# Kernel tuning notes

Hardware: AMD Instinct MI355X
Metric: run time of the kernel (lower is better)

The kernel has to match this reference:

```python
import jax, jax.numpy as jnp
import numpy as np

NUM_HEADS = 16
HEAD_SIZE = 64
D_MODEL = NUM_HEADS * HEAD_SIZE  # 1024


def setup_inputs() -> dict:
    key = jax.random.key(0)
    ks = jax.random.split(key, 12)
    B, S = 4, 2048
    q = jax.random.normal(ks[0], (B, S, D_MODEL), dtype=jnp.float32)
    k = jax.random.normal(ks[1], (B, S, D_MODEL), dtype=jnp.float32)
    v = jax.random.normal(ks[2], (B, S, D_MODEL), dtype=jnp.float32)
    w = jax.random.uniform(ks[3], (B, S), dtype=jnp.float32)
    scale = 1.0 / np.sqrt(D_MODEL)
    Wq = jax.random.normal(ks[4], (D_MODEL, D_MODEL), dtype=jnp.float32) * scale
    Wk = jax.random.normal(ks[5], (D_MODEL, D_MODEL), dtype=jnp.float32) * scale
    Wv = jax.random.normal(ks[6], (D_MODEL, D_MODEL), dtype=jnp.float32) * scale
    Wo = jax.random.normal(ks[7], (D_MODEL, D_MODEL), dtype=jnp.float32) * scale
    bq = jnp.zeros((D_MODEL,), jnp.float32)
    bk = jnp.zeros((D_MODEL,), jnp.float32)
    bv = jnp.zeros((D_MODEL,), jnp.float32)
    bo = jnp.zeros((D_MODEL,), jnp.float32)
    return {"q": q, "k": k, "v": v, "w": w,
            "Wq": Wq, "bq": bq, "Wk": Wk, "bk": bk,
            "Wv": Wv, "bv": bv, "Wo": Wo, "bo": bo}


def reference(q, k, v, w, Wq, bq, Wk, bk, Wv, bv, Wo, bo):
    B, S, _ = q.shape
    H, Dh = NUM_HEADS, HEAD_SIZE

    def split_heads(x):  # [B,S,D] -> [B,H,S,Dh]
        return x.reshape(B, -1, H, Dh).transpose(0, 2, 1, 3)

    q_h = split_heads(q @ Wq + bq)
    k_h = split_heads(k @ Wk + bk)
    v_h = split_heads(v @ Wv + bv)

    # [B,H,Sq,Sk]
    score = jnp.einsum('bhqd,bhkd->bhqk', q_h, k_h) / jnp.sqrt(
        jnp.asarray(Dh, jnp.float32))
    # weighted unnormalized softmax: exp(score)*w / sum (no max subtraction,
    # faithful to original)
    exp_score = jnp.exp(score) * w[:, None, None, :]
    attn = exp_score / (jnp.sum(exp_score, axis=-1, keepdims=True) + 1e-12)

    context = jnp.einsum('bhqk,bhkd->bhqd', attn, v_h)  # [B,H,S,Dh]
    context = context.transpose(0, 2, 1, 3).reshape(B, -1, H * Dh)
    return context @ Wo + bo
```

## Files before the change

### kernel.cpp

```cpp
#include <hip/hip_runtime.h>
#include <hip/hip_bf16.h>

typedef __bf16 bf16x8 __attribute__((ext_vector_type(8)));
typedef float f32x4 __attribute__((ext_vector_type(4)));
typedef float f32x8 __attribute__((ext_vector_type(8)));
typedef float f32x16 __attribute__((ext_vector_type(16)));
typedef unsigned short u16;
typedef unsigned int u32;

#define SB 4
#define SS 2048
#define SD 1024
#define SH 16
#define SDH 64

__device__ __forceinline__ u16 f2bf(float f) {
  union { float f; u32 u; } x; x.f = f;
  u32 r = (x.u + 0x7FFFu + ((x.u >> 16) & 1u)) >> 16;
  return (u16)r;
}

__device__ __forceinline__ void gl_lds16(const void* g, void* l) {
  __builtin_amdgcn_global_load_lds(
      (__attribute__((address_space(1))) void*)g,
      (__attribute__((address_space(3))) void*)l, 16, 0, 0);
}

__global__ void cast3_kernel(const float* __restrict__ q,
                             const float* __restrict__ k,
                             const float* __restrict__ v,
                             u32* __restrict__ oq, u32* __restrict__ ok,
                             u32* __restrict__ ov) {
  int sel = blockIdx.y;
  const float* in = (sel == 0) ? q : (sel == 1) ? k : v;
  u32* out = (sel == 0) ? oq : (sel == 1) ? ok : ov;
  int i = blockIdx.x * 256 + threadIdx.x;
  const float4* inp = (const float4*)in;
  float4 a = inp[2 * i], b = inp[2 * i + 1];
  uint4 o;
  asm("v_cvt_pk_bf16_f32 %0, %1, %2" : "=v"(o.x) : "v"(a.x), "v"(a.y));
  asm("v_cvt_pk_bf16_f32 %0, %1, %2" : "=v"(o.y) : "v"(a.z), "v"(a.w));
  asm("v_cvt_pk_bf16_f32 %0, %1, %2" : "=v"(o.z) : "v"(b.x), "v"(b.y));
  asm("v_cvt_pk_bf16_f32 %0, %1, %2" : "=v"(o.w) : "v"(b.z), "v"(b.w));
  ((uint4*)out)[i] = o;
}

__global__ void log2w_kernel(const float* __restrict__ w,
                             float* __restrict__ lwg) {
  int i = blockIdx.x * 256 + threadIdx.x;
  lwg[i] = __builtin_amdgcn_logf(w[i]);
}

__global__ void transpose_cast_kernel(const float* __restrict__ W0,
                                      const float* __restrict__ W1,
                                      const float* __restrict__ W2,
                                      const float* __restrict__ W3,
                                      u16* __restrict__ T0,
                                      u16* __restrict__ T1,
                                      u16* __restrict__ T2,
                                      u16* __restrict__ T3) {
  __shared__ float t[32][33];
  int z = blockIdx.z;
  const float* W = (z == 0) ? W0 : (z == 1) ? W1 : (z == 2) ? W2 : W3;
  u16* Wt = (z == 0) ? T0 : (z == 1) ? T1 : (z == 2) ? T2 : T3;
  int bx = blockIdx.x, by = blockIdx.y;
  int tx = threadIdx.x, ty = threadIdx.y;
#pragma unroll
  for (int j = 0; j < 32; j += 8)
    t[ty + j][tx] = W[(size_t)(by * 32 + ty + j) * SD + bx * 32 + tx];
  __syncthreads();
#pragma unroll
  for (int j = 0; j < 32; j += 8)
    Wt[(size_t)(bx * 32 + ty + j) * SD + by * 32 + tx] = f2bf(t[tx][ty + j]);
}

template <int MODE>
__global__ __launch_bounds__(256, 2)
void gemm_bt(const u16* __restrict__ A, const u16* __restrict__ Bt,
             const float* __restrict__ bias, void* __restrict__ Out,
             int M, int N, int K) {
  __shared__ u16 Asl[2][128 * 64];
  __shared__ u16 Bsl[2][128 * 64];
  const int ntile = N >> 7;
  int bid = blockIdx.x;
  bid = (bid & 7) * ((int)gridDim.x >> 3) + (bid >> 3);
  int m0 = (bid / ntile) * 128, n0 = (bid % ntile) * 128;
  int tid = threadIdx.x;
  int lane = tid & 63, wv = tid >> 6;
  int wr = wv >> 1, wc = wv & 1;

  auto stage = [&](int buf, int k0) {
#pragma unroll
    for (int it = 0; it < 4; ++it) {
      int c = tid + it * 256;
      int row = c >> 3, sl = c & 7;
      int ssl = sl ^ (row & 7);
      gl_lds16(A + (size_t)(m0 + row) * K + k0 + ssl * 8,
               (char*)&Asl[buf][0] + c * 16);
      gl_lds16(Bt + (size_t)(n0 + row) * K + k0 + ssl * 8,
               (char*)&Bsl[buf][0] + c * 16);
    }
  };

  f32x4 acc[4][4] = {};
  stage(0, 0);

  int nk = K >> 6;
  for (int kt = 0; kt < nk; ++kt) {
    int buf = kt & 1;
    if (kt + 1 < nk) {
      stage(buf ^ 1, (kt + 1) << 6);
      asm volatile("s_waitcnt vmcnt(8) lgkmcnt(0)" ::: "memory");
    } else {
      asm volatile("s_waitcnt vmcnt(0) lgkmcnt(0)" ::: "memory");
    }
    __builtin_amdgcn_s_barrier();
#pragma unroll
    for (int kk = 0; kk < 2; ++kk) {
      bf16x8 af[4], bfr[4];
#pragma unroll
      for (int i = 0; i < 4; ++i) {
        int ar = wr * 64 + i * 16 + (lane & 15);
        int abyt = (ar * 128 + (kk * 32 + (lane >> 4) * 8) * 2) ^
                   ((ar & 7) << 4);
        af[i] = *(const bf16x8*)((const char*)&Asl[buf][0] + abyt);
        int br = wc * 64 + i * 16 + (lane & 15);
        int bbyt = (br * 128 + (kk * 32 + (lane >> 4) * 8) * 2) ^
                   ((br & 7) << 4);
        bfr[i] = *(const bf16x8*)((const char*)&Bsl[buf][0] + bbyt);
      }
#pragma unroll
      for (int i = 0; i < 4; ++i)
#pragma unroll
        for (int j = 0; j < 4; ++j)
          acc[i][j] = __builtin_amdgcn_mfma_f32_16x16x32_bf16(
              af[i], bfr[j], acc[i][j], 0, 0, 0);
    }
    __builtin_amdgcn_s_barrier();
  }

  int cg = lane >> 4, cc = lane & 15;
#pragma unroll
  for (int i = 0; i < 4; ++i) {
#pragma unroll
    for (int j = 0; j < 4; ++j) {
#pragma unroll
      for (int r = 0; r < 4; ++r) {
        int m = m0 + wr * 64 + i * 16 + cg * 4 + r;
        int n = n0 + wc * 64 + j * 16 + cc;
        float val = acc[i][j][r];
        if (MODE == 0) {
          val = (val + bias[n]) * 0.18033688011112042f;
          int b = m >> 11, s = m & 2047, h = n >> 6, dh = n & 63;
          ((u16*)Out)[((size_t)((b * SH + h) * SS + s) << 6) + dh] = f2bf(val);
        } else if (MODE == 1) {
          val += bias[n];
          int b = m >> 11, s = m & 2047, h = n >> 6, dh = n & 63;
          size_t off = ((size_t)(b * SH + h) << 17) + ((size_t)(s >> 5) << 11) +
                       ((size_t)(dh >> 4) << 9) +
                       ((size_t)((s & 31) | ((dh & 8) << 2)) << 3) + (dh & 7);
          ((u16*)Out)[off] = f2bf(val);
        } else if (MODE == 2) {
          val += bias[m];
          int h = m >> 6, dh = m & 63, b = n >> 11, s = n & 2047;
          size_t off = ((size_t)(b * SH + h) << 17) + ((size_t)(s >> 4) << 10) +
                       ((size_t)(dh >> 5) << 9) +
                       ((size_t)(((s >> 3) & 1) * 32 + (dh & 31)) << 3) +
                       (s & 7);
          ((u16*)Out)[off] = f2bf(val);
        } else {
          val += bias[n];
          ((float*)Out)[(size_t)m * N + n] = val;
        }
      }
    }
  }
}

__global__ __launch_bounds__(256, 4)
void attn_kernel(const u16* __restrict__ Qh, const u16* __restrict__ Kf,
                 const u16* __restrict__ Vf, const float* __restrict__ lwg,
                 u16* __restrict__ Ctx) {
  __shared__ u16 Kl[2][4096];
  __shared__ u16 Vl[2][4096];
  __shared__ float lwl[SS];

  int bid = blockIdx.x;
  int swz = (bid & 7) * 128 + (bid >> 3);
  int bh = swz >> 4;
  int qt = swz & 15;
  int b = bh >> 4, hh = bh & 15;
  int q0 = qt * 128;
  int tid = threadIdx.x, lane = tid & 63, qw = tid >> 6;
  int ql = lane & 31, h = lane >> 5;
  const size_t basebh = (size_t)bh * (SS * SDH);
  const char* Ksrc = (const char*)(Kf + basebh);
  const char* Vsrc = (const char*)(Vf + basebh);

  {
    const float4* src = (const float4*)(lwg + b * SS);
    float4 r0 = src[tid];
    float4 r1 = src[tid + 256];
    ((float4*)lwl)[tid] = r0;
    ((float4*)lwl)[tid + 256] = r1;
  }

  bf16x8 qf[4];
  {
    const u16* qp = Qh + basebh + (size_t)(q0 + qw * 32 + ql) * SDH + h * 8;
#pragma unroll
    for (int st = 0; st < 4; ++st) qf[st] = *(const bf16x8*)(qp + st * 16);
  }

  auto stageK = [&](int s, int t) {
    const char* p = Ksrc + (size_t)t * 8192;
    gl_lds16(p + tid * 16, (char*)&Kl[s][0] + tid * 16);
    gl_lds16(p + 4096 + tid * 16, (char*)&Kl[s][0] + 4096 + tid * 16);
  };
  auto stageV = [&](int s, int t) {
    const char* p = Vsrc + (size_t)t * 8192;
    gl_lds16(p + tid * 16, (char*)&Vl[s][0] + tid * 16);
    gl_lds16(p + 4096 + tid * 16, (char*)&Vl[s][0] + 4096 + tid * 16);
  };

  f32x16 ctx0 = {}, ctx1 = {};
  float rs = 0.f;
  u32 pk[8][2];

  auto qk = [&](int t) {
    const char* Ks = (const char*)&Kl[t & 1][0];
    int kvb = t * 64;
#pragma unroll
    for (int kt = 0; kt < 2; ++kt) {
      bf16x8 kf[4];
#pragma unroll
      for (int st = 0; st < 4; ++st)
        kf[st] = *(const bf16x8*)(Ks + (kt * 4 + st) * 1024 + lane * 16);
      const float* lb = lwl + kvb + kt * 32 + h * 4;
      f32x4 l0 = *(const f32x4*)(lb);
      f32x4 l1 = *(const f32x4*)(lb + 8);
      f32x4 l2 = *(const f32x4*)(lb + 16);
      f32x4 l3 = *(const f32x4*)(lb + 24);
      f32x8 lo = __builtin_shufflevector(l0, l1, 0, 1, 2, 3, 4, 5, 6, 7);
      f32x8 hi = __builtin_shufflevector(l2, l3, 0, 1, 2, 3, 4, 5, 6, 7);
      f32x16 sc = __builtin_shufflevector(lo, hi, 0, 1, 2, 3, 4, 5, 6, 7, 8,
                                          9, 10, 11, 12, 13, 14, 15);
      __builtin_amdgcn_s_setprio(1);
#pragma unroll
      for (int st = 0; st < 4; ++st)
        sc = __builtin_amdgcn_mfma_f32_32x32x16_bf16(kf[st], qf[st], sc,
                                                     0, 0, 0);
      __builtin_amdgcn_s_setprio(0);
#pragma unroll
      for (int e2 = 0; e2 < 4; ++e2) {
        float v0 = __builtin_amdgcn_exp2f(sc[e2 * 4 + 0]);
        float v1 = __builtin_amdgcn_exp2f(sc[e2 * 4 + 1]);
        float v2 = __builtin_amdgcn_exp2f(sc[e2 * 4 + 2]);
        float v3 = __builtin_amdgcn_exp2f(sc[e2 * 4 + 3]);
        rs += (v0 + v1) + (v2 + v3);
        u32 p0, p1;
        asm("v_cvt_pk_bf16_f32 %0, %1, %2" : "=v"(p0) : "v"(v0), "v"(v1));
        asm("v_cvt_pk_bf16_f32 %0, %1, %2" : "=v"(p1) : "v"(v2), "v"(v3));
        pk[kt * 4 + e2][0] = p0;
        pk[kt * 4 + e2][1] = p1;
      }
    }
  };

  auto pv = [&](int t) {
    const char* Vs = (const char*)&Vl[t & 1][0];
#pragma unroll
    for (int ksl = 0; ksl < 4; ++ksl) {
      bf16x8 vf0 = *(const bf16x8*)(Vs + (ksl * 2 + 0) * 1024 + lane * 16);
      bf16x8 vf1 = *(const bf16x8*)(Vs + (ksl * 2 + 1) * 1024 + lane * 16);
      u32 d0 = pk[2 * ksl][0], d1 = pk[2 * ksl][1];
      u32 s0 = pk[2 * ksl + 1][0], s1 = pk[2 * ksl + 1][1];
      asm("v_permlane32_swap_b32 %0, %1" : "+v"(d0), "+v"(s0));
      asm("v_permlane32_swap_b32 %0, %1" : "+v"(d1), "+v"(s1));
      union { u32 uu[4]; bf16x8 v; } pa;
      pa.uu[0] = d0; pa.uu[1] = d1; pa.uu[2] = s0; pa.uu[3] = s1;
      __builtin_amdgcn_s_setprio(1);
      ctx0 = __builtin_amdgcn_mfma_f32_32x32x16_bf16(pa.v, vf0, ctx0, 0, 0, 0);
      ctx1 = __builtin_amdgcn_mfma_f32_32x32x16_bf16(pa.v, vf1, ctx1, 0, 0, 0);
      __builtin_amdgcn_s_setprio(0);
    }
  };

  stageK(0, 0);
  stageV(0, 0);
  asm volatile("s_waitcnt lgkmcnt(0)" ::: "memory");
  __builtin_amdgcn_s_barrier();

  for (int t = 0; t < 31; ++t) {
    asm volatile("s_waitcnt vmcnt(2)" ::: "memory");
    __builtin_amdgcn_s_barrier();
    stageK((t + 1) & 1, t + 1);
    stageV((t + 1) & 1, t + 1);
    qk(t);
    asm volatile("s_waitcnt vmcnt(4)" ::: "memory");
    pv(t);
  }
  asm volatile("s_waitcnt vmcnt(2)" ::: "memory");
  __builtin_amdgcn_s_barrier();
  qk(31);
  asm volatile("s_waitcnt vmcnt(0)" ::: "memory");
  pv(31);

  rs += __shfl_xor(rs, 32, 64);
  float rinv = 1.0f / (rs + 1e-12f);
#pragma unroll
  for (int reg = 0; reg < 16; ++reg) {
    int qrow = (reg & 3) + 8 * (reg >> 2) + 4 * h;
    float ri = __shfl(rinv, qrow, 64);
    int srow = q0 + qw * 32 + qrow;
    size_t base = ((size_t)(b * SS + srow) << 10) + hh * SDH;
    Ctx[base + ql] = f2bf(ctx0[reg] * ri);
    Ctx[base + 32 + ql] = f2bf(ctx1[reg] * ri);
  }
}

extern "C" void kernel_launch(void* const* d_in, const int* in_sizes, int n_in,
                              void* d_out, int out_size, void* d_ws,
                              size_t ws_size, hipStream_t stream) {
  const float* q = (const float*)d_in[0];
  const float* k = (const float*)d_in[1];
  const float* v = (const float*)d_in[2];
  const float* w = (const float*)d_in[3];
  const float* Wq = (const float*)d_in[4];
  const float* bq = (const float*)d_in[5];
  const float* Wk = (const float*)d_in[6];
  const float* bk = (const float*)d_in[7];
  const float* Wv = (const float*)d_in[8];
  const float* bv = (const float*)d_in[9];
  const float* Wo = (const float*)d_in[10];
  const float* bo = (const float*)d_in[11];
  float* out = (float*)d_out;

  char* ws = (char*)d_ws;
  const size_t SZ = (size_t)8192 * 1024 * 2;
  u16* qb = (u16*)(ws);
  u16* kb = (u16*)(ws + SZ);
  u16* vb = (u16*)(ws + 2 * SZ);
  u16* WqT = (u16*)(ws + 3 * SZ);
  u16* WkT = WqT + 1024 * 1024;
  u16* WvT = WkT + 1024 * 1024;
  u16* WoT = WvT + 1024 * 1024;
  u16* Qh = (u16*)(ws + 3 * SZ + (size_t)4 * 1024 * 1024 * 2);
  u16* Kf = Qh + (size_t)8192 * 1024;
  u16* Vf = Kf + (size_t)8192 * 1024;
  float* lwg = (float*)(ws + 3 * SZ + (size_t)4 * 1024 * 1024 * 2 +
                        (size_t)3 * 8192 * 1024 * 2);
  u16* Ctx = qb;

  cast3_kernel<<<dim3(4096, 3), 256, 0, stream>>>(q, k, v, (u32*)qb,
                                                  (u32*)kb, (u32*)vb);
  log2w_kernel<<<32, 256, 0, stream>>>(w, lwg);
  dim3 tb(32, 8), tg(32, 32, 4);
  transpose_cast_kernel<<<tg, tb, 0, stream>>>(Wq, Wk, Wv, Wo,
                                               WqT, WkT, WvT, WoT);

  gemm_bt<0><<<512, 256, 0, stream>>>(qb, WqT, bq, Qh, 8192, 1024, 1024);
  gemm_bt<1><<<512, 256, 0, stream>>>(kb, WkT, bk, Kf, 8192, 1024, 1024);
  gemm_bt<2><<<512, 256, 0, stream>>>(WvT, vb, bv, Vf, 1024, 8192, 1024);

  attn_kernel<<<1024, 256, 0, stream>>>(Qh, Kf, Vf, lwg, Ctx);

  gemm_bt<3><<<512, 256, 0, stream>>>(Ctx, WoT, bo, out, 8192, 1024, 1024);
}
```

Measured before the change: 214.3 us.

## Software-pipeline attention: overlap softmax of tile t with PV of tile t-1

Restructures the attention loop so QK for tile t runs, then the exp/convert softmax for tile t is interleaved with the PV MFMAs of tile t-1, using double-buffered probability registers and a triple-buffered V LDS ring. The goal is to hide transcendental and VALU latency under matrix-core work. In exchange it uses more LDS (an extra V buffer) and more registers, and launch bounds drop to 3 blocks per CU, which lowers occupancy.

New measurement: 219.4 us. +2.4%, slower.

```diff
diff --git a/kernel.cpp b/kernel.cpp
--- a/kernel.cpp
+++ b/kernel.cpp
@@ -177,12 +177,12 @@
   }
 }
 
-__global__ __launch_bounds__(256, 4)
+__global__ __launch_bounds__(256, 3)
 void attn_kernel(const u16* __restrict__ Qh, const u16* __restrict__ Kf,
                  const u16* __restrict__ Vf, const float* __restrict__ lwg,
                  u16* __restrict__ Ctx) {
   __shared__ u16 Kl[2][4096];
-  __shared__ u16 Vl[2][4096];
+  __shared__ u16 Vl[3][4096];
   __shared__ float lwl[SS];
 
   int bid = blockIdx.x;
@@ -225,10 +225,9 @@
 
   f32x16 ctx0 = {}, ctx1 = {};
   float rs = 0.f;
-  u32 pk[8][2];
-
-  auto qk = [&](int t) {
-    const char* Ks = (const char*)&Kl[t & 1][0];
+  u32 pkA[8][2], pkB[8][2];
+
+  auto qk = [&](const char* Ks, int t, f32x16& s0v, f32x16& s1v) {
     int kvb = t * 64;
 #pragma unroll
     for (int kt = 0; kt < 2; ++kt) {
@@ -251,30 +250,38 @@
         sc = __builtin_amdgcn_mfma_f32_32x32x16_bf16(kf[st], qf[st], sc,
                                                      0, 0, 0);
       __builtin_amdgcn_s_setprio(0);
-#pragma unroll
-      for (int e2 = 0; e2 < 4; ++e2) {
-        float v0 = __builtin_amdgcn_exp2f(sc[e2 * 4 + 0]);
-        float v1 = __builtin_amdgcn_exp2f(sc[e2 * 4 + 1]);
-        float v2 = __builtin_amdgcn_exp2f(sc[e2 * 4 + 2]);
-        float v3 = __builtin_amdgcn_exp2f(sc[e2 * 4 + 3]);
-        rs += (v0 + v1) + (v2 + v3);
-        u32 p0, p1;
-        asm("v_cvt_pk_bf16_f32 %0, %1, %2" : "=v"(p0) : "v"(v0), "v"(v1));
-        asm("v_cvt_pk_bf16_f32 %0, %1, %2" : "=v"(p1) : "v"(v2), "v"(v3));
-        pk[kt * 4 + e2][0] = p0;
-        pk[kt * 4 + e2][1] = p1;
-      }
-    }
-  };
-
-  auto pv = [&](int t) {
-    const char* Vs = (const char*)&Vl[t & 1][0];
+      if (kt == 0) s0v = sc; else s1v = sc;
+    }
+  };
+
+#define SM_SLICE(sidx, scv)                                                 \
+  {                                                                         \
+    float v0 = __builtin_amdgcn_exp2f((scv)[((sidx) & 3) * 4 + 0]);         \
+    float v1 = __builtin_amdgcn_exp2f((scv)[((sidx) & 3) * 4 + 1]);         \
+    float v2 = __builtin_amdgcn_exp2f((scv)[((sidx) & 3) * 4 + 2]);         \
+    float v3 = __builtin_amdgcn_exp2f((scv)[((sidx) & 3) * 4 + 3]);         \
+    rs += (v0 + v1) + (v2 + v3);                                            \
+    asm("v_cvt_pk_bf16_f32 %0, %1, %2"                                      \
+        : "=v"(pkN[sidx][0]) : "v"(v0), "v"(v1));                           \
+    asm("v_cvt_pk_bf16_f32 %0, %1, %2"                                      \
+        : "=v"(pkN[sidx][1]) : "v"(v2), "v"(v3));                           \
+  }
+
+  auto region2 = [&](f32x16& s0v, f32x16& s1v, u32 (&pkN)[8][2],
+                     u32 (&pkO)[8][2], const char* Vs) {
 #pragma unroll
     for (int ksl = 0; ksl < 4; ++ksl) {
       bf16x8 vf0 = *(const bf16x8*)(Vs + (ksl * 2 + 0) * 1024 + lane * 16);
       bf16x8 vf1 = *(const bf16x8*)(Vs + (ksl * 2 + 1) * 1024 + lane * 16);
-      u32 d0 = pk[2 * ksl][0], d1 = pk[2 * ksl][1];
-      u32 s0 = pk[2 * ksl + 1][0], s1 = pk[2 * ksl + 1][1];
+      if (ksl < 2) {
+        SM_SLICE(2 * ksl + 0, s0v);
+        SM_SLICE(2 * ksl + 1, s0v);
+      } else {
+        SM_SLICE(2 * ksl + 0, s1v);
+        SM_SLICE(2 * ksl + 1, s1v);
+      }
+      u32 d0 = pkO[2 * ksl][0], d1 = pkO[2 * ksl][1];
+      u32 s0 = pkO[2 * ksl + 1][0], s1 = pkO[2 * ksl + 1][1];
       asm("v_permlane32_swap_b32 %0, %1" : "+v"(d0), "+v"(s0));
       asm("v_permlane32_swap_b32 %0, %1" : "+v"(d1), "+v"(s1));
       union { u32 uu[4]; bf16x8 v; } pa;
@@ -286,25 +293,60 @@
     }
   };
 
+  auto smx_only = [&](f32x16& s0v, f32x16& s1v, u32 (&pkN)[8][2]) {
+#pragma unroll
+    for (int sidx = 0; sidx < 8; ++sidx) {
+      if (sidx < 4) SM_SLICE(sidx, s0v) else SM_SLICE(sidx, s1v);
+    }
+  };
+  auto pv_only = [&](u32 (&pkO)[8][2], const char* Vs) {
+#pragma unroll
+    for (int ksl = 0; ksl < 4; ++ksl) {
+      bf16x8 vf0 = *(const bf16x8*)(Vs + (ksl * 2 + 0) * 1024 + lane * 16);
+      bf16x8 vf1 = *(const bf16x8*)(Vs + (ksl * 2 + 1) * 1024 + lane * 16);
+      u32 d0 = pkO[2 * ksl][0], d1 = pkO[2 * ksl][1];
+      u32 s0 = pkO[2 * ksl + 1][0], s1 = pkO[2 * ksl + 1][1];
+      asm("v_permlane32_swap_b32 %0, %1" : "+v"(d0), "+v"(s0));
+      asm("v_permlane32_swap_b32 %0, %1" : "+v"(d1), "+v"(s1));
+      union { u32 uu[4]; bf16x8 v; } pa;
+      pa.uu[0] = d0; pa.uu[1] = d1; pa.uu[2] = s0; pa.uu[3] = s1;
+      ctx0 = __builtin_amdgcn_mfma_f32_32x32x16_bf16(pa.v, vf0, ctx0, 0, 0, 0);
+      ctx1 = __builtin_amdgcn_mfma_f32_32x32x16_bf16(pa.v, vf1, ctx1, 0, 0, 0);
+    }
+  };
+
+  f32x16 sc0, sc1;
+
   stageK(0, 0);
   stageV(0, 0);
-  asm volatile("s_waitcnt lgkmcnt(0)" ::: "memory");
+  asm volatile("s_waitcnt vmcnt(2) lgkmcnt(0)" ::: "memory");
   __builtin_amdgcn_s_barrier();
-
-  for (int t = 0; t < 31; ++t) {
+  stageK(1, 1);
+  stageV(1, 1);
+  qk((const char*)&Kl[0][0], 0, sc0, sc1);
+  smx_only(sc0, sc1, pkA);
+
+  for (int t = 1; t <= 29; t += 2) {
     asm volatile("s_waitcnt vmcnt(2)" ::: "memory");
     __builtin_amdgcn_s_barrier();
     stageK((t + 1) & 1, t + 1);
-    stageV((t + 1) & 1, t + 1);
-    qk(t);
-    asm volatile("s_waitcnt vmcnt(4)" ::: "memory");
-    pv(t);
+    stageV((t + 1) % 3, t + 1);
+    qk((const char*)&Kl[t & 1][0], t, sc0, sc1);
+    region2(sc0, sc1, pkB, pkA, (const char*)&Vl[(t - 1) % 3][0]);
+    asm volatile("s_waitcnt vmcnt(2)" ::: "memory");
+    __builtin_amdgcn_s_barrier();
+    stageK((t + 2) & 1, t + 2);
+    stageV((t + 2) % 3, t + 2);
+    qk((const char*)&Kl[(t + 1) & 1][0], t + 1, sc0, sc1);
+    region2(sc0, sc1, pkA, pkB, (const char*)&Vl[t % 3][0]);
   }
   asm volatile("s_waitcnt vmcnt(2)" ::: "memory");
   __builtin_amdgcn_s_barrier();
-  qk(31);
+  qk((const char*)&Kl[1][0], 31, sc0, sc1);
+  region2(sc0, sc1, pkB, pkA, (const char*)&Vl[30 % 3][0]);
   asm volatile("s_waitcnt vmcnt(0)" ::: "memory");
-  pv(31);
+  pv_only(pkB, (const char*)&Vl[31 % 3][0]);
+#undef SM_SLICE
 
   rs += __shfl_xor(rs, 32, 64);
   float rinv = 1.0f / (rs + 1e-12f);
```

## Merge prep kernels into one launch and halve GEMM K-tile for occupancy

Applied to the files above, without the earlier changes.

Folds the cast, log-weight and weight transpose-cast kernels into a single prep kernel dispatched by block index, removing two launches. The GEMM K-tile shrinks from 64 to 32, halving LDS per block, and launch bounds are raised to allow three blocks per CU. A new swizzle packs two rows per 128-byte LDS line. The trade is more K iterations and barriers per tile in exchange for higher occupancy and fewer launches.

After: 222.6 us. +3.9%, slower.

```diff
diff --git a/kernel.cpp b/kernel.cpp
--- a/kernel.cpp
+++ b/kernel.cpp
@@ -26,61 +26,60 @@
       (__attribute__((address_space(3))) void*)l, 16, 0, 0);
 }
 
-__global__ void cast3_kernel(const float* __restrict__ q,
-                             const float* __restrict__ k,
-                             const float* __restrict__ v,
-                             u32* __restrict__ oq, u32* __restrict__ ok,
-                             u32* __restrict__ ov) {
-  int sel = blockIdx.y;
-  const float* in = (sel == 0) ? q : (sel == 1) ? k : v;
-  u32* out = (sel == 0) ? oq : (sel == 1) ? ok : ov;
-  int i = blockIdx.x * 256 + threadIdx.x;
-  const float4* inp = (const float4*)in;
-  float4 a = inp[2 * i], b = inp[2 * i + 1];
-  uint4 o;
-  asm("v_cvt_pk_bf16_f32 %0, %1, %2" : "=v"(o.x) : "v"(a.x), "v"(a.y));
-  asm("v_cvt_pk_bf16_f32 %0, %1, %2" : "=v"(o.y) : "v"(a.z), "v"(a.w));
-  asm("v_cvt_pk_bf16_f32 %0, %1, %2" : "=v"(o.z) : "v"(b.x), "v"(b.y));
-  asm("v_cvt_pk_bf16_f32 %0, %1, %2" : "=v"(o.w) : "v"(b.z), "v"(b.w));
-  ((uint4*)out)[i] = o;
-}
-
-__global__ void log2w_kernel(const float* __restrict__ w,
-                             float* __restrict__ lwg) {
-  int i = blockIdx.x * 256 + threadIdx.x;
-  lwg[i] = __builtin_amdgcn_logf(w[i]);
-}
-
-__global__ void transpose_cast_kernel(const float* __restrict__ W0,
-                                      const float* __restrict__ W1,
-                                      const float* __restrict__ W2,
-                                      const float* __restrict__ W3,
-                                      u16* __restrict__ T0,
-                                      u16* __restrict__ T1,
-                                      u16* __restrict__ T2,
-                                      u16* __restrict__ T3) {
+__global__ void prep_kernel(const float* __restrict__ q,
+                            const float* __restrict__ k,
+                            const float* __restrict__ v,
+                            u32* __restrict__ oq, u32* __restrict__ ok,
+                            u32* __restrict__ ov,
+                            const float* __restrict__ w,
+                            float* __restrict__ lwg,
+                            const float* __restrict__ W0,
+                            const float* __restrict__ W1,
+                            const float* __restrict__ W2,
+                            const float* __restrict__ W3,
+                            u16* __restrict__ T0, u16* __restrict__ T1,
+                            u16* __restrict__ T2, u16* __restrict__ T3) {
   __shared__ float t[32][33];
-  int z = blockIdx.z;
-  const float* W = (z == 0) ? W0 : (z == 1) ? W1 : (z == 2) ? W2 : W3;
-  u16* Wt = (z == 0) ? T0 : (z == 1) ? T1 : (z == 2) ? T2 : T3;
-  int bx = blockIdx.x, by = blockIdx.y;
-  int tx = threadIdx.x, ty = threadIdx.y;
-#pragma unroll
-  for (int j = 0; j < 32; j += 8)
-    t[ty + j][tx] = W[(size_t)(by * 32 + ty + j) * SD + bx * 32 + tx];
-  __syncthreads();
-#pragma unroll
-  for (int j = 0; j < 32; j += 8)
-    Wt[(size_t)(bx * 32 + ty + j) * SD + by * 32 + tx] = f2bf(t[tx][ty + j]);
+  int bid = blockIdx.x, tid = threadIdx.x;
+  if (bid < 12288) {
+    int sel = bid >> 12;
+    int i = (bid & 4095) * 256 + tid;
+    const float* in = (sel == 0) ? q : (sel == 1) ? k : v;
+    u32* out = (sel == 0) ? oq : (sel == 1) ? ok : ov;
+    const float4* inp = (const float4*)in;
+    float4 a = inp[2 * i], b = inp[2 * i + 1];
+    uint4 o;
+    asm("v_cvt_pk_bf16_f32 %0, %1, %2" : "=v"(o.x) : "v"(a.x), "v"(a.y));
+    asm("v_cvt_pk_bf16_f32 %0, %1, %2" : "=v"(o.y) : "v"(a.z), "v"(a.w));
+    asm("v_cvt_pk_bf16_f32 %0, %1, %2" : "=v"(o.z) : "v"(b.x), "v"(b.y));
+    asm("v_cvt_pk_bf16_f32 %0, %1, %2" : "=v"(o.w) : "v"(b.z), "v"(b.w));
+    ((uint4*)out)[i] = o;
+  } else if (bid < 16384) {
+    int local = bid - 12288;
+    int z = local >> 10, by = (local >> 5) & 31, bx = local & 31;
+    const float* W = (z == 0) ? W0 : (z == 1) ? W1 : (z == 2) ? W2 : W3;
+    u16* Wt = (z == 0) ? T0 : (z == 1) ? T1 : (z == 2) ? T2 : T3;
+    int tx = tid & 31, ty = tid >> 5;
+#pragma unroll
+    for (int j = 0; j < 32; j += 8)
+      t[ty + j][tx] = W[(size_t)(by * 32 + ty + j) * SD + bx * 32 + tx];
+    __syncthreads();
+#pragma unroll
+    for (int j = 0; j < 32; j += 8)
+      Wt[(size_t)(bx * 32 + ty + j) * SD + by * 32 + tx] = f2bf(t[tx][ty + j]);
+  } else {
+    int i = (bid - 16384) * 256 + tid;
+    lwg[i] = __builtin_amdgcn_logf(w[i]);
+  }
 }
 
 template <int MODE>
-__global__ __launch_bounds__(256, 2)
+__global__ __launch_bounds__(256, 3)
 void gemm_bt(const u16* __restrict__ A, const u16* __restrict__ Bt,
              const float* __restrict__ bias, void* __restrict__ Out,
              int M, int N, int K) {
-  __shared__ u16 Asl[2][128 * 64];
-  __shared__ u16 Bsl[2][128 * 64];
+  __shared__ u16 Asl[2][4096];
+  __shared__ u16 Bsl[2][4096];
   const int ntile = N >> 7;
   int bid = blockIdx.x;
   bid = (bid & 7) * ((int)gridDim.x >> 3) + (bid >> 3);
@@ -91,13 +90,15 @@
 
   auto stage = [&](int buf, int k0) {
 #pragma unroll
-    for (int it = 0; it < 4; ++it) {
+    for (int it = 0; it < 2; ++it) {
       int c = tid + it * 256;
-      int row = c >> 3, sl = c & 7;
-      int ssl = sl ^ (row & 7);
-      gl_lds16(A + (size_t)(m0 + row) * K + k0 + ssl * 8,
+      int r = c >> 3, p = c & 7;
+      int qs = p ^ (r & 7);
+      int a = 2 * r + (qs >> 2);
+      int ks = qs & 3;
+      gl_lds16(A + (size_t)(m0 + a) * K + k0 + ks * 8,
                (char*)&Asl[buf][0] + c * 16);
-      gl_lds16(Bt + (size_t)(n0 + row) * K + k0 + ssl * 8,
+      gl_lds16(Bt + (size_t)(n0 + a) * K + k0 + ks * 8,
                (char*)&Bsl[buf][0] + c * 16);
     }
   };
@@ -105,37 +106,35 @@
   f32x4 acc[4][4] = {};
   stage(0, 0);
 
-  int nk = K >> 6;
+  int nk = K >> 5;
   for (int kt = 0; kt < nk; ++kt) {
     int buf = kt & 1;
     if (kt + 1 < nk) {
-      stage(buf ^ 1, (kt + 1) << 6);
-      asm volatile("s_waitcnt vmcnt(8) lgkmcnt(0)" ::: "memory");
+      stage(buf ^ 1, (kt + 1) << 5);
+      asm volatile("s_waitcnt vmcnt(4) lgkmcnt(0)" ::: "memory");
     } else {
       asm volatile("s_waitcnt vmcnt(0) lgkmcnt(0)" ::: "memory");
     }
     __builtin_amdgcn_s_barrier();
-#pragma unroll
-    for (int kk = 0; kk < 2; ++kk) {
-      bf16x8 af[4], bfr[4];
-#pragma unroll
-      for (int i = 0; i < 4; ++i) {
-        int ar = wr * 64 + i * 16 + (lane & 15);
-        int abyt = (ar * 128 + (kk * 32 + (lane >> 4) * 8) * 2) ^
-                   ((ar & 7) << 4);
-        af[i] = *(const bf16x8*)((const char*)&Asl[buf][0] + abyt);
-        int br = wc * 64 + i * 16 + (lane & 15);
-        int bbyt = (br * 128 + (kk * 32 + (lane >> 4) * 8) * 2) ^
-                   ((br & 7) << 4);
-        bfr[i] = *(const bf16x8*)((const char*)&Bsl[buf][0] + bbyt);
-      }
-#pragma unroll
-      for (int i = 0; i < 4; ++i)
-#pragma unroll
-        for (int j = 0; j < 4; ++j)
-          acc[i][j] = __builtin_amdgcn_mfma_f32_16x16x32_bf16(
-              af[i], bfr[j], acc[i][j], 0, 0, 0);
-    }
+    bf16x8 af[4], bfr[4];
+    int s = lane >> 4;
+#pragma unroll
+    for (int i = 0; i < 4; ++i) {
+      int ar = wr * 64 + i * 16 + (lane & 15);
+      int abyt = (ar >> 1) * 128 +
+                 (((((ar & 1) << 2) | s) ^ ((ar >> 1) & 7)) << 4);
+      af[i] = *(const bf16x8*)((const char*)&Asl[buf][0] + abyt);
+      int br = wc * 64 + i * 16 + (lane & 15);
+      int bbyt = (br >> 1) * 128 +
+                 (((((br & 1) << 2) | s) ^ ((br >> 1) & 7)) << 4);
+      bfr[i] = *(const bf16x8*)((const char*)&Bsl[buf][0] + bbyt);
+    }
+#pragma unroll
+    for (int i = 0; i < 4; ++i)
+#pragma unroll
+      for (int j = 0; j < 4; ++j)
+        acc[i][j] = __builtin_amdgcn_mfma_f32_16x16x32_bf16(
+            af[i], bfr[j], acc[i][j], 0, 0, 0);
     __builtin_amdgcn_s_barrier();
   }
 
@@ -151,22 +150,24 @@
         float val = acc[i][j][r];
         if (MODE == 0) {
           val = (val + bias[n]) * 0.18033688011112042f;
-          int b = m >> 11, s = m & 2047, h = n >> 6, dh = n & 63;
-          ((u16*)Out)[((size_t)((b * SH + h) * SS + s) << 6) + dh] = f2bf(val);
+          int b = m >> 11, s2 = m & 2047, h = n >> 6, dh = n & 63;
+          ((u16*)Out)[((size_t)((b * SH + h) * SS + s2) << 6) + dh] =
+              f2bf(val);
         } else if (MODE == 1) {
           val += bias[n];
-          int b = m >> 11, s = m & 2047, h = n >> 6, dh = n & 63;
-          size_t off = ((size_t)(b * SH + h) << 17) + ((size_t)(s >> 5) << 11) +
-                       ((size_t)(dh >> 4) << 9) +
-                       ((size_t)((s & 31) | ((dh & 8) << 2)) << 3) + (dh & 7);
+          int b = m >> 11, s2 = m & 2047, h = n >> 6, dh = n & 63;
+          size_t off = ((size_t)(b * SH + h) << 17) +
+                       ((size_t)(s2 >> 5) << 11) + ((size_t)(dh >> 4) << 9) +
+                       ((size_t)((s2 & 31) | ((dh & 8) << 2)) << 3) +
+                       (dh & 7);
           ((u16*)Out)[off] = f2bf(val);
         } else if (MODE == 2) {
           val += bias[m];
-          int h = m >> 6, dh = m & 63, b = n >> 11, s = n & 2047;
-          size_t off = ((size_t)(b * SH + h) << 17) + ((size_t)(s >> 4) << 10) +
-                       ((size_t)(dh >> 5) << 9) +
-                       ((size_t)(((s >> 3) & 1) * 32 + (dh & 31)) << 3) +
-                       (s & 7);
+          int h = m >> 6, dh = m & 63, b = n >> 11, s2 = n & 2047;
+          size_t off = ((size_t)(b * SH + h) << 17) +
+                       ((size_t)(s2 >> 4) << 10) + ((size_t)(dh >> 5) << 9) +
+                       ((size_t)(((s2 >> 3) & 1) * 32 + (dh & 31)) << 3) +
+                       (s2 & 7);
           ((u16*)Out)[off] = f2bf(val);
         } else {
           val += bias[n];
@@ -352,12 +353,9 @@
                         (size_t)3 * 8192 * 1024 * 2);
   u16* Ctx = qb;
 
-  cast3_kernel<<<dim3(4096, 3), 256, 0, stream>>>(q, k, v, (u32*)qb,
-                                                  (u32*)kb, (u32*)vb);
-  log2w_kernel<<<32, 256, 0, stream>>>(w, lwg);
-  dim3 tb(32, 8), tg(32, 32, 4);
-  transpose_cast_kernel<<<tg, tb, 0, stream>>>(Wq, Wk, Wv, Wo,
-                                               WqT, WkT, WvT, WoT);
+  prep_kernel<<<16416, 256, 0, stream>>>(q, k, v, (u32*)qb, (u32*)kb,
+                                         (u32*)vb, w, lwg, Wq, Wk, Wv, Wo,
+                                         WqT, WkT, WvT, WoT);
 
   gemm_bt<0><<<512, 256, 0, stream>>>(qb, WqT, bq, Qh, 8192, 1024, 1024);
   gemm_bt<1><<<512, 256, 0, stream>>>(kb, WkT, bk, Kf, 8192, 1024, 1024);
```
